# Kernel optimization log

Measured on AMD Instinct MI355X. Metric: run time of the kernel, lower is better.

The kernel has to match this reference:

```python
import jax, jax.numpy as jnp
import numpy as np

N = 20000; E = 320000; IN = 128; H = 6; C = 64; HC = H * C; NC = 16; NG = 64


def _gatv2(x, src, dst, wl, bl, wr, br, att, bias, heads, out_c, concat):
    # PyG GATv2Conv (eval mode, share_weights=False, negative_slope=0.2)
    n = x.shape[0]
    xl = (x @ wl + bl).reshape(n, heads, out_c)   # source-side transform
    xr = (x @ wr + br).reshape(n, heads, out_c)   # target-side transform
    # edge-wise attention logits: leaky_relu(x_l[j] + x_r[i]) . att
    e = jnp.einsum('ehc,hc->eh', jax.nn.leaky_relu(xl[src] + xr[dst], 0.2), att)
    # segment softmax over incoming edges of each target node
    emax = jax.ops.segment_max(e, dst, num_segments=n)
    a = jnp.exp(e - emax[dst])
    denom = jax.ops.segment_sum(a, dst, num_segments=n)
    alpha = a / (denom[dst] + 1e-16)
    out = jax.ops.segment_sum(xl[src] * alpha[:, :, None], dst, num_segments=n)
    out = out.reshape(n, heads * out_c) if concat else out.mean(axis=1)
    return out + bias


def setup_inputs() -> dict:
    key = jax.random.key(0)
    ks = jax.random.split(key, 32)
    s = 0.05
    inp = {}
    inp['x'] = jax.random.normal(ks[0], (N, IN), jnp.float32)
    inp['edge_index'] = jax.random.randint(ks[1], (2, E), 0, N, dtype=jnp.int32)
    inp['batch'] = jnp.sort(jax.random.randint(ks[2], (N,), 0, NG, dtype=jnp.int32))
    # input projection (input_dim != hidden_dim * n_heads)
    inp['inp_w'] = jax.random.normal(ks[3], (IN, HC), jnp.float32) * s
    inp['inp_b'] = jnp.zeros((HC,), jnp.float32)
    # layer 0: IN -> (H, C), concat
    inp['l0_wl'] = jax.random.normal(ks[4], (IN, HC), jnp.float32) * s
    inp['l0_bl'] = jnp.zeros((HC,), jnp.float32)
    inp['l0_wr'] = jax.random.normal(ks[5], (IN, HC), jnp.float32) * s
    inp['l0_br'] = jnp.zeros((HC,), jnp.float32)
    inp['l0_att'] = jax.random.normal(ks[6], (H, C), jnp.float32) * s
    inp['l0_bias'] = jnp.zeros((HC,), jnp.float32)
    # layer 1: HC -> (H, C), concat
    inp['l1_wl'] = jax.random.normal(ks[7], (HC, HC), jnp.float32) * s
    inp['l1_bl'] = jnp.zeros((HC,), jnp.float32)
    inp['l1_wr'] = jax.random.normal(ks[8], (HC, HC), jnp.float32) * s
    inp['l1_br'] = jnp.zeros((HC,), jnp.float32)
    inp['l1_att'] = jax.random.normal(ks[9], (H, C), jnp.float32) * s
    inp['l1_bias'] = jnp.zeros((HC,), jnp.float32)
    # layer 2: HC -> (1, C), no concat (mean over the single head)
    inp['l2_wl'] = jax.random.normal(ks[10], (HC, C), jnp.float32) * s
    inp['l2_bl'] = jnp.zeros((C,), jnp.float32)
    inp['l2_wr'] = jax.random.normal(ks[11], (HC, C), jnp.float32) * s
    inp['l2_br'] = jnp.zeros((C,), jnp.float32)
    inp['l2_att'] = jax.random.normal(ks[12], (1, C), jnp.float32) * s
    inp['l2_bias'] = jnp.zeros((C,), jnp.float32)
    # residual projection HC -> C at the last layer (bias-free Linear)
    inp['res_w'] = jax.random.normal(ks[13], (HC, C), jnp.float32) * s
    # dense head: Linear(C,C) + BatchNorm1d(eval) + ReLU + Linear(C,NC)
    inp['d1_w'] = jax.random.normal(ks[14], (C, C), jnp.float32) * s
    inp['d1_b'] = jnp.zeros((C,), jnp.float32)
    inp['bn_g'] = jnp.ones((C,), jnp.float32)
    inp['bn_b'] = jnp.zeros((C,), jnp.float32)
    inp['bn_m'] = jnp.zeros((C,), jnp.float32)
    inp['bn_v'] = jnp.ones((C,), jnp.float32)
    inp['d2_w'] = jax.random.normal(ks[15], (C, NC), jnp.float32) * s
    inp['d2_b'] = jnp.zeros((NC,), jnp.float32)
    return inp


def reference(x, edge_index, batch, inp_w, inp_b,
              l0_wl, l0_bl, l0_wr, l0_br, l0_att, l0_bias,
              l1_wl, l1_bl, l1_wr, l1_br, l1_att, l1_bias,
              l2_wl, l2_bl, l2_wr, l2_br, l2_att, l2_bias,
              res_w, d1_w, d1_b, bn_g, bn_b, bn_m, bn_v, d2_w, d2_b):
    n = x.shape[0]
    sl = jnp.arange(n, dtype=edge_index.dtype)           # self-loops (PyG default)
    src = jnp.concatenate([edge_index[0], sl])
    dst = jnp.concatenate([edge_index[1], sl])
    x_res = x @ inp_w + inp_b
    h = jax.nn.elu(_gatv2(x, src, dst, l0_wl, l0_bl, l0_wr, l0_br, l0_att, l0_bias, H, C, True)) + x_res
    x_res = h
    h = jax.nn.elu(_gatv2(h, src, dst, l1_wl, l1_bl, l1_wr, l1_br, l1_att, l1_bias, H, C, True)) + x_res
    x_res = h
    h = jax.nn.elu(_gatv2(h, src, dst, l2_wl, l2_bl, l2_wr, l2_br, l2_att, l2_bias, 1, C, False)) + x_res @ res_w
    pooled = jax.ops.segment_sum(h, batch, num_segments=NG)
    z = pooled @ d1_w + d1_b
    z = (z - bn_m) / jnp.sqrt(bn_v + 1e-5) * bn_g + bn_b  # BatchNorm1d eval
    z = jax.nn.relu(z) @ d2_w + d2_b
    return h, z
```

## Files before the change

### kernel.cpp

```cpp
#include <hip/hip_runtime.h>
#include <hip/hip_bf16.h>
#include <math.h>

#define NN 20000
#define EE 320000
#define IND 128
#define HH 6
#define CC 64
#define HCC 384
#define NCC 16
#define NGG 64

typedef __bf16 bf16x8 __attribute__((ext_vector_type(8)));
typedef float f32x4 __attribute__((ext_vector_type(4)));
typedef float f32x2 __attribute__((ext_vector_type(2)));
typedef unsigned short ushort_t;
typedef unsigned int uint_t;

#define LOG2E 1.44269504088896f

__device__ inline ushort_t f2bf(float f) {
    union { float f; uint_t u; } x; x.f = f;
    uint_t r = (x.u + 0x7FFF + ((x.u >> 16) & 1)) >> 16;
    return (ushort_t)r;
}
__device__ inline void bf8cvt2(uint4 v, f32x2* f) {
    union { uint_t u; float x; } a, b;
    a.u = v.x << 16; b.u = v.x & 0xFFFF0000u; f[0] = (f32x2){a.x, b.x};
    a.u = v.y << 16; b.u = v.y & 0xFFFF0000u; f[1] = (f32x2){a.x, b.x};
    a.u = v.z << 16; b.u = v.z & 0xFFFF0000u; f[2] = (f32x2){a.x, b.x};
    a.u = v.w << 16; b.u = v.w & 0xFFFF0000u; f[3] = (f32x2){a.x, b.x};
}

template <int CTRL>
__device__ inline float dppadd(float x) {
    int y = __builtin_amdgcn_mov_dpp(__builtin_bit_cast(int, x), CTRL, 0xF, 0xF, true);
    return x + __builtin_bit_cast(float, y);
}

__device__ inline void load_lds16(const ushort_t* g, ushort_t* l) {
    __builtin_amdgcn_global_load_lds(
        (const __attribute__((address_space(1))) void*)g,
        (__attribute__((address_space(3))) void*)l, 16, 0, 0);
}


__global__ void zero_init_kernel(int* counts, int* srcs_tail, int n) {
    int t = blockIdx.x * blockDim.x + threadIdx.x;
    if (t < n) counts[t] = 0;
    if (t < 8) srcs_tail[t] = 0;
}

__global__ void count_kernel(const int* __restrict__ ei, int* __restrict__ counts, int E) {
    int t = blockIdx.x * blockDim.x + threadIdx.x;
    if (t < E) atomicAdd(&counts[ei[E + t]], 1);
}

__global__ void scan_kernel(const int* __restrict__ counts, int* __restrict__ offsets,
                            int* __restrict__ cursor, int n) {
    __shared__ int part[1024];
    int t = threadIdx.x;
    int per = (n + 1023) / 1024;
    int base = t * per;
    int sum = 0;
    for (int j = 0; j < per; ++j) {
        int idx = base + j;
        if (idx < n) sum += counts[idx] + 1;
    }
    part[t] = sum;
    __syncthreads();
    for (int off = 1; off < 1024; off <<= 1) {
        int v = (t >= off) ? part[t - off] : 0;
        __syncthreads();
        part[t] += v;
        __syncthreads();
    }
    int run = (t == 0) ? 0 : part[t - 1];
    for (int j = 0; j < per; ++j) {
        int idx = base + j;
        if (idx < n) {
            int deg = counts[idx] + 1;
            offsets[idx] = run;
            cursor[idx] = run;
            run += deg;
        }
    }
    if (t == 1023) offsets[n] = part[1023];
}

__global__ void fill_kernel(const int* __restrict__ ei, int* __restrict__ cursor,
                            int* __restrict__ srcs, int E, int n) {
    int t = blockIdx.x * blockDim.x + threadIdx.x;
    if (t < E) {
        int s = ei[t];
        int d = ei[E + t];
        int slot = atomicAdd(&cursor[d], 1);
        srcs[slot] = s;
    } else if (t < E + n) {
        int i = t - E;
        int slot = atomicAdd(&cursor[i], 1);
        srcs[slot] = i;
    }
}

#define WBIG (1152 * IND)
#define WC1 (768 * HCC)
#define WC2 (192 * HCC)
#define XB_N (NN * IND)
#define PREP_TOTAL (WBIG + WC1 + WC2 + XB_N + 1152 + 768 + 192)

__global__ void prep_kernel(const float* __restrict__ x, const float* __restrict__ inp_w,
    const float* __restrict__ l0wl, const float* __restrict__ l0wr,
    const float* __restrict__ l1wl, const float* __restrict__ l1wr,
    const float* __restrict__ l2wl, const float* __restrict__ l2wr,
    const float* __restrict__ resw,
    const float* __restrict__ inp_b,
    const float* __restrict__ l0bl, const float* __restrict__ l0br,
    const float* __restrict__ l1bl, const float* __restrict__ l1br,
    const float* __restrict__ l2bl, const float* __restrict__ l2br,
    ushort_t* wBig, ushort_t* wC1, ushort_t* wC2, ushort_t* xb,
    float* bBig, float* bC1, float* bC2)
{
    int i = blockIdx.x * blockDim.x + threadIdx.x;
    if (i >= PREP_TOTAL) return;
    if (i < WBIG) {
        int col = i >> 7, k = i & 127;
        float v;
        if (col < 384)      v = inp_w[k * 384 + col];
        else if (col < 768) v = l0wl[k * 384 + (col - 384)];
        else                v = l0wr[k * 384 + (col - 768)];
        wBig[i] = f2bf(v); return;
    }
    i -= WBIG;
    if (i < WC1) {
        int col = i / 384, k = i - col * 384;
        float v = col < 384 ? l1wl[k * 384 + col] : l1wr[k * 384 + (col - 384)];
        wC1[i] = f2bf(v); return;
    }
    i -= WC1;
    if (i < WC2) {
        int col = i / 384, k = i - col * 384;
        float v;
        if (col < 64)       v = resw[k * 64 + col];
        else if (col < 128) v = l2wl[k * 64 + (col - 64)];
        else                v = l2wr[k * 64 + (col - 128)];
        wC2[i] = f2bf(v); return;
    }
    i -= WC2;
    if (i < XB_N) { xb[i] = f2bf(x[i]); return; }
    i -= XB_N;
    if (i < 1152) {
        float v;
        if (i < 384)      v = inp_b[i];
        else if (i < 768) v = l0bl[i - 384];
        else              v = l0br[i - 768];
        bBig[i] = v; return;
    }
    i -= 1152;
    if (i < 768) { bC1[i] = i < 384 ? l1bl[i] : l1br[i - 384]; return; }
    i -= 768;
    if (i < 192) {
        float v;
        if (i < 64)       v = 0.0f;
        else if (i < 128) v = l2bl[i - 64];
        else              v = l2br[i - 128];
        bC2[i] = v; return;
    }
}

__global__ __launch_bounds__(256) void gemm_mfma(
    const ushort_t* __restrict__ A, const ushort_t* __restrict__ BT,
    const float* __restrict__ bias,
    float* __restrict__ Cf, ushort_t* __restrict__ Cb1, int ld1,
    ushort_t* __restrict__ Cb2, int ld2, int split,
    int M, int N, int K)
{
    __shared__ ushort_t Bs[2][2][128 * 32];
    int t = threadIdx.x;
    int w = t >> 6, L = t & 63;
    int m0 = blockIdx.x * 128, n0 = blockIdx.y * 128;
    int q = L >> 4, r16 = L & 15;

    f32x4 acc[2][8];
#pragma unroll
    for (int a = 0; a < 2; ++a)
#pragma unroll
        for (int b = 0; b < 8; ++b) acc[a][b] = (f32x4){0.f, 0.f, 0.f, 0.f};

    int lr = L >> 2;
    int lc = ((L & 3) ^ ((lr >> 1) & 3)) * 8;
    int rB0 = min(n0 + w * 32 + lr, N - 1);
    int rB1 = min(n0 + w * 32 + 16 + lr, N - 1);
    const ushort_t* gB0 = BT + (size_t)rB0 * K + lc;
    const ushort_t* gB1 = BT + (size_t)rB1 * K + lc;
    int oB0 = (w * 32) * 32;
    int oB1 = (w * 32 + 16) * 32;

    int rA0 = min(m0 + w * 32 + r16, M - 1);
    int rA1 = min(m0 + w * 32 + 16 + r16, M - 1);
    const ushort_t* pA0 = A + (size_t)rA0 * K + q * 8;
    const ushort_t* pA1 = A + (size_t)rA1 * K + q * 8;

    int sw = (q ^ ((r16 >> 1) & 3)) * 8;

    load_lds16(gB0, &Bs[0][0][oB0]);
    load_lds16(gB1, &Bs[0][0][oB1]);
    load_lds16(gB0 + 32, &Bs[0][1][oB0]);
    load_lds16(gB1 + 32, &Bs[0][1][oB1]);
    gB0 += 64; gB1 += 64;
    bf16x8 a0 = *(const bf16x8*)pA0;
    bf16x8 a2 = *(const bf16x8*)(pA0 + 32);
    bf16x8 a1 = *(const bf16x8*)pA1;
    bf16x8 a3 = *(const bf16x8*)(pA1 + 32);
    pA0 += 64; pA1 += 64;

    int buf = 0;
    for (int k0 = 0; k0 < K; k0 += 64) {
        __syncthreads();
        bool more = (k0 + 64 < K);
        if (more) {
            int nb = buf ^ 1;
            load_lds16(gB0, &Bs[nb][0][oB0]);
            load_lds16(gB1, &Bs[nb][0][oB1]);
            load_lds16(gB0 + 32, &Bs[nb][1][oB0]);
            load_lds16(gB1 + 32, &Bs[nb][1][oB1]);
            gB0 += 64; gB1 += 64;
        }
        bf16x8 na0, na1, na2, na3;
        if (more) {
            na0 = *(const bf16x8*)pA0;
            na2 = *(const bf16x8*)(pA0 + 32);
            na1 = *(const bf16x8*)pA1;
            na3 = *(const bf16x8*)(pA1 + 32);
            pA0 += 64; pA1 += 64;
        }
#pragma unroll
        for (int ct = 0; ct < 8; ++ct) {
            bf16x8 blo = *(const bf16x8*)&Bs[buf][0][(ct * 16 + r16) * 32 + sw];
            bf16x8 bhi = *(const bf16x8*)&Bs[buf][1][(ct * 16 + r16) * 32 + sw];
            acc[0][ct] = __builtin_amdgcn_mfma_f32_16x16x32_bf16(blo, a0, acc[0][ct], 0, 0, 0);
            acc[1][ct] = __builtin_amdgcn_mfma_f32_16x16x32_bf16(blo, a1, acc[1][ct], 0, 0, 0);
            acc[0][ct] = __builtin_amdgcn_mfma_f32_16x16x32_bf16(bhi, a2, acc[0][ct], 0, 0, 0);
            acc[1][ct] = __builtin_amdgcn_mfma_f32_16x16x32_bf16(bhi, a3, acc[1][ct], 0, 0, 0);
        }
        if (more) { a0 = na0; a1 = na1; a2 = na2; a3 = na3; }
        buf ^= 1;
    }
#pragma unroll
    for (int rt = 0; rt < 2; ++rt) {
        int row = m0 + w * 32 + rt * 16 + r16;
        if (row >= M) continue;
#pragma unroll
        for (int ct = 0; ct < 8; ++ct) {
            int colb = n0 + ct * 16 + q * 4;
            if (colb >= N) continue;
            float4 bv = *(const float4*)(bias + colb);
            float v0 = acc[rt][ct][0] + bv.x;
            float v1 = acc[rt][ct][1] + bv.y;
            float v2 = acc[rt][ct][2] + bv.z;
            float v3 = acc[rt][ct][3] + bv.w;
            if (colb < split) {
                if (Cf) {
                    *(float4*)(Cf + (size_t)row * ld1 + colb) = make_float4(v0, v1, v2, v3);
                } else {
                    uint2 pk;
                    pk.x = (uint_t)f2bf(v0) | ((uint_t)f2bf(v1) << 16);
                    pk.y = (uint_t)f2bf(v2) | ((uint_t)f2bf(v3) << 16);
                    *(uint2*)(Cb1 + (size_t)row * ld1 + colb) = pk;
                }
            } else {
                uint2 pk;
                pk.x = (uint_t)f2bf(v0) | ((uint_t)f2bf(v1) << 16);
                pk.y = (uint_t)f2bf(v2) | ((uint_t)f2bf(v3) << 16);
                *(uint2*)(Cb2 + (size_t)row * ld2 + (colb - split)) = pk;
            }
        }
    }
}

__global__ __launch_bounds__(128) void gat6_kernel(
    const ushort_t* __restrict__ cat, const float* __restrict__ att,
    const float* __restrict__ bias, const ushort_t* __restrict__ resB,
    ushort_t* __restrict__ outB,
    const int* __restrict__ offsets, const int* __restrict__ srcs, int n)
{
    int wid = (blockIdx.x * blockDim.x + threadIdx.x) >> 6;
    if (wid >= n) return;
    int lane = threadIdx.x & 63;
    int h = lane >> 3, c8 = lane & 7;
    bool hv = h < HH;
    int off = h * 64 + c8 * 8;
    int offL = hv ? off : off - 384;
    int i = wid;
    int beg = offsets[i], end = offsets[i + 1];
    int deg = end - beg;
    int P = (deg + 1) >> 1;

    f32x2 xr2[4], att2[4];
    {
        uint4 v = *(const uint4*)(cat + (size_t)i * 768 + 384 + offL);
        bf8cvt2(v, xr2);
    }
#pragma unroll
    for (int j = 0; j < 4; ++j)
        att2[j] = (f32x2){att[offL + 2 * j] * LOG2E, att[offL + 2 * j + 1] * LOG2E};

    float s = 0.0f;
    f32x2 acc2[4];
#pragma unroll
    for (int j = 0; j < 4; ++j) acc2[j] = (f32x2){0.f, 0.f};

    int ia0 = srcs[beg], ib0 = srcs[beg + 1];
    uint4 cA = *(const uint4*)(cat + (size_t)ia0 * 768 + offL);
    uint4 cB = *(const uint4*)(cat + (size_t)ib0 * 768 + offL);
    int iA1 = srcs[beg + 2], iB1 = srcs[beg + 3];

    for (int p = 0; p < P; ++p) {
        uint4 nA = cA, nB = cB;
        bool pre = (p + 1 < P);
        if (pre) {
            nA = *(const uint4*)(cat + (size_t)iA1 * 768 + offL);
            nB = *(const uint4*)(cat + (size_t)iB1 * 768 + offL);
            iA1 = srcs[beg + 2 * p + 4];
            iB1 = srcs[beg + 2 * p + 5];
        }
        f32x2 xlA[4], xlB[4];
        bf8cvt2(cA, xlA);
        bf8cvt2(cB, xlB);
        f32x2 pA2 = (f32x2){0.f, 0.f}, pB2 = (f32x2){0.f, 0.f};
#pragma unroll
        for (int j = 0; j < 4; ++j) {
            f32x2 ta = xlA[j] + xr2[j];
            ta = __builtin_elementwise_max(ta, ta * 0.2f);
            pA2 += ta * att2[j];
            f32x2 tb = xlB[j] + xr2[j];
            tb = __builtin_elementwise_max(tb, tb * 0.2f);
            pB2 += tb * att2[j];
        }
        float pA = pA2.x + pA2.y, pB = pB2.x + pB2.y;
        pA = dppadd<0xB1>(pA);
        pB = dppadd<0xB1>(pB);
        pA = dppadd<0x4E>(pA);
        pB = dppadd<0x4E>(pB);
        pA = dppadd<0x141>(pA);
        pB = dppadd<0x141>(pB);
        float wA = __builtin_amdgcn_exp2f(pA);
        float wB = (2 * p + 1 < deg) ? __builtin_amdgcn_exp2f(pB) : 0.0f;
        s += wA + wB;
        f32x2 wA2 = (f32x2){wA, wA}, wB2 = (f32x2){wB, wB};
#pragma unroll
        for (int j = 0; j < 4; ++j) {
            acc2[j] += wA2 * xlA[j];
            acc2[j] += wB2 * xlB[j];
        }
        cA = nA; cB = nB;
    }

    if (hv) {
        float inv = 1.0f / (s + 1e-16f);
        size_t ob = (size_t)i * HCC + off;
        uint4 rv = *(const uint4*)(resB + ob);
        f32x2 rr[4];
        bf8cvt2(rv, rr);
        ushort_t u[8];
#pragma unroll
        for (int j = 0; j < 4; ++j) {
            float v0 = acc2[j].x * inv + bias[off + 2 * j];
            float v1 = acc2[j].y * inv + bias[off + 2 * j + 1];
            v0 = v0 > 0.0f ? v0 : expm1f(v0);
            v1 = v1 > 0.0f ? v1 : expm1f(v1);
            u[2 * j]     = f2bf(v0 + rr[j].x);
            u[2 * j + 1] = f2bf(v1 + rr[j].y);
        }
        *(uint4*)(outB + ob) = *(uint4*)u;
    }
}

__global__ __launch_bounds__(128) void gat1_kernel(
    const ushort_t* __restrict__ cat, const float* __restrict__ att,
    const float* __restrict__ bias, const float* __restrict__ res,
    float* __restrict__ out,
    const int* __restrict__ offsets, const int* __restrict__ srcs, int n)
{
    int wid = (blockIdx.x * blockDim.x + threadIdx.x) >> 6;
    if (wid >= n) return;
    int lane = threadIdx.x & 63;
    int e8 = lane >> 3, c8 = lane & 7;
    int i = wid;
    int beg = offsets[i], end = offsets[i + 1];

    f32x2 xr2[4], att2[4];
    {
        uint4 v = *(const uint4*)(cat + (size_t)i * 128 + 64 + c8 * 8);
        bf8cvt2(v, xr2);
    }
#pragma unroll
    for (int j = 0; j < 4; ++j)
        att2[j] = (f32x2){att[c8 * 8 + 2 * j] * LOG2E, att[c8 * 8 + 2 * j + 1] * LOG2E};

    float s = 0.0f;
    f32x2 acc2[4];
#pragma unroll
    for (int j = 0; j < 4; ++j) acc2[j] = (f32x2){0.f, 0.f};

    const uint4 z = make_uint4(0u, 0u, 0u, 0u);
    int p = beg + e8;
    bool val = p < end;
    int sj = val ? srcs[p] : i;
    uint4 v = *(const uint4*)(cat + (size_t)sj * 128 + c8 * 8);

    for (int p0 = beg; p0 < end; p0 += 8) {
        uint4 nv = z;
        bool nval = false;
        if (p0 + 8 < end) {
            int np = p0 + 8 + e8;
            nval = np < end;
            int nsj = nval ? srcs[np] : i;
            nv = *(const uint4*)(cat + (size_t)nsj * 128 + c8 * 8);
        }
        f32x2 xl[4];
        bf8cvt2(v, xl);
        f32x2 pp2 = (f32x2){0.f, 0.f};
#pragma unroll
        for (int j = 0; j < 4; ++j) {
            f32x2 tv = xl[j] + xr2[j];
            tv = __builtin_elementwise_max(tv, tv * 0.2f);
            pp2 += tv * att2[j];
        }
        float partial = pp2.x + pp2.y;
        partial = dppadd<0xB1>(partial);
        partial = dppadd<0x4E>(partial);
        partial = dppadd<0x141>(partial);
        float wE = val ? __builtin_amdgcn_exp2f(partial) : 0.0f;
        s += wE;
        f32x2 w2 = (f32x2){wE, wE};
#pragma unroll
        for (int j = 0; j < 4; ++j) acc2[j] += w2 * xl[j];
        v = nv;
        val = nval;
    }

    s = dppadd<0x140>(s);
    s += __shfl_xor(s, 16, 64);
    s += __shfl_xor(s, 32, 64);
#pragma unroll
    for (int j = 0; j < 4; ++j) {
        acc2[j].x += __shfl_xor(acc2[j].x, 8, 64);
        acc2[j].y += __shfl_xor(acc2[j].y, 8, 64);
        acc2[j].x += __shfl_xor(acc2[j].x, 16, 64);
        acc2[j].y += __shfl_xor(acc2[j].y, 16, 64);
        acc2[j].x += __shfl_xor(acc2[j].x, 32, 64);
        acc2[j].y += __shfl_xor(acc2[j].y, 32, 64);
    }
    if (e8 == 0) {
        float inv = 1.0f / (s + 1e-16f);
        size_t ob = (size_t)i * CC + c8 * 8;
        float4 r0 = *(const float4*)(res + ob);
        float4 r1 = *(const float4*)(res + ob + 4);
        float rr[8] = {r0.x, r0.y, r0.z, r0.w, r1.x, r1.y, r1.z, r1.w};
        float av[8] = {acc2[0].x, acc2[0].y, acc2[1].x, acc2[1].y,
                       acc2[2].x, acc2[2].y, acc2[3].x, acc2[3].y};
#pragma unroll
        for (int j = 0; j < 8; ++j) {
            float v2 = av[j] * inv + bias[c8 * 8 + j];
            v2 = v2 > 0.0f ? v2 : expm1f(v2);
            av[j] = v2 + rr[j];
        }
        *(float4*)(out + ob) = make_float4(av[0], av[1], av[2], av[3]);
        *(float4*)(out + ob + 4) = make_float4(av[4], av[5], av[6], av[7]);
    }
}

__global__ __launch_bounds__(256) void pool_kernel(const float* __restrict__ h,
                                                   const int* __restrict__ batch,
                                                   float* __restrict__ pooled, int n) {
    int g = blockIdx.x;
    int t = threadIdx.x;
    int w = t >> 6, lane = t & 63;
    int lo = 0, hi = n;
    while (lo < hi) { int mid = (lo + hi) >> 1; if (batch[mid] < g) lo = mid + 1; else hi = mid; }
    int start = lo;
    int hi2 = n;
    while (lo < hi2) { int mid = (lo + hi2) >> 1; if (batch[mid] < g + 1) lo = mid + 1; else hi2 = mid; }
    int endd = lo;
    float acc = 0.0f;
    for (int r = start + w; r < endd; r += 4)
        acc += h[(size_t)r * 64 + lane];
    __shared__ float red[4][64];
    red[w][lane] = acc;
    __syncthreads();
    if (w == 0)
        pooled[g * 64 + lane] = red[0][lane] + red[1][lane] + red[2][lane] + red[3][lane];
}

__global__ void head_kernel(const float* __restrict__ pooled,
                            const float* __restrict__ d1w, const float* __restrict__ d1b,
                            const float* __restrict__ bng, const float* __restrict__ bnb,
                            const float* __restrict__ bnm, const float* __restrict__ bnv,
                            const float* __restrict__ d2w, const float* __restrict__ d2b,
                            float* __restrict__ zout) {
    __shared__ float z1[64 * 64];
    int t = threadIdx.x;
    for (int idx = t; idx < 64 * 64; idx += 256) {
        int r = idx >> 6, c = idx & 63;
        float acc = d1b[c];
        for (int k = 0; k < 64; ++k) acc += pooled[r * 64 + k] * d1w[k * 64 + c];
        acc = (acc - bnm[c]) / sqrtf(bnv[c] + 1e-5f) * bng[c] + bnb[c];
        z1[idx] = acc > 0.0f ? acc : 0.0f;
    }
    __syncthreads();
    for (int idx = t; idx < 64 * NCC; idx += 256) {
        int r = idx >> 4, c = idx & 15;
        float acc = d2b[c];
        for (int k = 0; k < 64; ++k) acc += z1[r * 64 + k] * d2w[k * NCC + c];
        zout[idx] = acc;
    }
}


extern "C" void kernel_launch(void* const* d_in, const int* in_sizes, int n_in,
                              void* d_out, int out_size, void* d_ws, size_t ws_size,
                              hipStream_t stream) {
    const int N = NN, E = EE, C = CC, HC = HCC, NG = NGG;
    const int EN = E + N;

    const float* x     = (const float*)d_in[0];
    const int*   ei    = (const int*)d_in[1];
    const int*   batch = (const int*)d_in[2];
    const float* inp_w = (const float*)d_in[3];
    const float* inp_b = (const float*)d_in[4];
    const float* l0_wl = (const float*)d_in[5];
    const float* l0_bl = (const float*)d_in[6];
    const float* l0_wr = (const float*)d_in[7];
    const float* l0_br = (const float*)d_in[8];
    const float* l0_att = (const float*)d_in[9];
    const float* l0_bias = (const float*)d_in[10];
    const float* l1_wl = (const float*)d_in[11];
    const float* l1_bl = (const float*)d_in[12];
    const float* l1_wr = (const float*)d_in[13];
    const float* l1_br = (const float*)d_in[14];
    const float* l1_att = (const float*)d_in[15];
    const float* l1_bias = (const float*)d_in[16];
    const float* l2_wl = (const float*)d_in[17];
    const float* l2_bl = (const float*)d_in[18];
    const float* l2_wr = (const float*)d_in[19];
    const float* l2_br = (const float*)d_in[20];
    const float* l2_att = (const float*)d_in[21];
    const float* l2_bias = (const float*)d_in[22];
    const float* res_w = (const float*)d_in[23];
    const float* d1_w = (const float*)d_in[24];
    const float* d1_b = (const float*)d_in[25];
    const float* bn_g = (const float*)d_in[26];
    const float* bn_b = (const float*)d_in[27];
    const float* bn_m = (const float*)d_in[28];
    const float* bn_v = (const float*)d_in[29];
    const float* d2_w = (const float*)d_in[30];
    const float* d2_b = (const float*)d_in[31];

    float* out = (float*)d_out;

    char* ws = (char*)d_ws;
    size_t off = 0;
    auto alloc = [&](size_t bytes) -> void* {
        void* p = ws + off;
        off += (bytes + 255) & ~(size_t)255;
        return p;
    };
    ushort_t* bufH_b  = (ushort_t*)alloc((size_t)N * HC * 2);
    ushort_t* cat01_b = (ushort_t*)alloc((size_t)N * 768 * 2 + 2048);
    ushort_t* xres_b  = (ushort_t*)alloc((size_t)N * HC * 2);
    ushort_t* cat2_b  = (ushort_t*)alloc((size_t)N * 128 * 2);
    float*    bufRes  = (float*)alloc((size_t)N * C * 4);
    ushort_t* xb      = (ushort_t*)alloc((size_t)N * IND * 2);
    ushort_t* wBig    = (ushort_t*)alloc((size_t)WBIG * 2);
    ushort_t* wC1     = (ushort_t*)alloc((size_t)WC1 * 2);
    ushort_t* wC2     = (ushort_t*)alloc((size_t)WC2 * 2);
    float*    bBig    = (float*)alloc((size_t)1152 * 4);
    float*    bC1     = (float*)alloc((size_t)768 * 4);
    float*    bC2     = (float*)alloc((size_t)192 * 4);
    int*      counts  = (int*)alloc((size_t)N * 4);
    int*      cursor  = (int*)alloc((size_t)N * 4);
    int*      offsets = (int*)alloc((size_t)(N + 1) * 4);
    int*      srcs    = (int*)alloc((size_t)(EN + 8) * 4);
    float*    pooled  = (float*)alloc((size_t)NG * C * 4);

    zero_init_kernel<<<(N + 255) / 256, 256, 0, stream>>>(counts, srcs + EN, N);
    count_kernel<<<(E + 255) / 256, 256, 0, stream>>>(ei, counts, E);
    scan_kernel<<<1, 1024, 0, stream>>>(counts, offsets, cursor, N);
    fill_kernel<<<(EN + 255) / 256, 256, 0, stream>>>(ei, cursor, srcs, E, N);
    prep_kernel<<<(PREP_TOTAL + 255) / 256, 256, 0, stream>>>(
        x, inp_w, l0_wl, l0_wr, l1_wl, l1_wr, l2_wl, l2_wr, res_w,
        inp_b, l0_bl, l0_br, l1_bl, l1_br, l2_bl, l2_br,
        wBig, wC1, wC2, xb, bBig, bC1, bC2);

    dim3 blk(256);
    int mtiles = (N + 127) / 128;
    dim3 gblk(128);
    int gatBlocks = (N * 64 + 127) / 128;

    gemm_mfma<<<dim3(mtiles, 9), blk, 0, stream>>>(xb, wBig, bBig,
        nullptr, xres_b, HC, cat01_b, 768, 384, N, 1152, IND);
    gat6_kernel<<<gatBlocks, gblk, 0, stream>>>(cat01_b, l0_att, l0_bias,
                                                xres_b, bufH_b, offsets, srcs, N);
    gemm_mfma<<<dim3(mtiles, 6), blk, 0, stream>>>(bufH_b, wC1, bC1,
        nullptr, nullptr, 0, cat01_b, 768, 0, N, 768, HC);
    gat6_kernel<<<gatBlocks, gblk, 0, stream>>>(cat01_b, l1_att, l1_bias,
                                                bufH_b, bufH_b, offsets, srcs, N);
    gemm_mfma<<<dim3(mtiles, 2), blk, 0, stream>>>(bufH_b, wC2, bC2,
        bufRes, nullptr, C, cat2_b, 128, 64, N, 192, HC);
    gat1_kernel<<<gatBlocks, gblk, 0, stream>>>(cat2_b, l2_att, l2_bias,
                                                bufRes, out, offsets, srcs, N);
    pool_kernel<<<NG, 256, 0, stream>>>(out, batch, pooled, N);
    head_kernel<<<1, 256, 0, stream>>>(pooled, d1_w, d1_b, bn_g, bn_b, bn_m, bn_v,
                                       d2_w, d2_b, out + (size_t)N * C);
}
```

Baseline: 429.9 us.

## Add 256-row multi-N-tile GEMM, precompute byte offsets, LDS-buffered scan

Adds a new 512-thread GEMM kernel that covers 256 rows per block and loops over several 128-column tiles, so each block reuses its A rows across column tiles and fewer blocks are launched for the first two projections. The fill kernel now stores source indices pre-scaled to byte offsets in two separate arrays, one per gather row stride, which removes the multiply in the gather loops. Edge offsets are loaded through readfirstlane so they live in scalar registers. The scan kernel stages the counts in LDS and writes offsets with coalesced accesses. In exchange it writes a second index array, uses a large LDS buffer in the scan, and runs fewer, heavier GEMM blocks that could lower occupancy.

```diff
diff --git a/kernel.cpp b/kernel.cpp
--- a/kernel.cpp
+++ b/kernel.cpp
@@ -45,10 +45,10 @@
 }
 
 
-__global__ void zero_init_kernel(int* counts, int* srcs_tail, int n) {
+__global__ void zero_init_kernel(int* counts, int* s6_tail, int* s1_tail, int n) {
     int t = blockIdx.x * blockDim.x + threadIdx.x;
     if (t < n) counts[t] = 0;
-    if (t < 8) srcs_tail[t] = 0;
+    if (t < 8) { s6_tail[t] = 0; s1_tail[t] = 0; }
 }
 
 __global__ void count_kernel(const int* __restrict__ ei, int* __restrict__ counts, int E) {
@@ -56,16 +56,20 @@
     if (t < E) atomicAdd(&counts[ei[E + t]], 1);
 }
 
-__global__ void scan_kernel(const int* __restrict__ counts, int* __restrict__ offsets,
-                            int* __restrict__ cursor, int n) {
+__global__ __launch_bounds__(1024) void scan_kernel(
+    const int* __restrict__ counts, int* __restrict__ offsets,
+    int* __restrict__ cursor, int n) {
+    __shared__ int buf[NN];
     __shared__ int part[1024];
     int t = threadIdx.x;
+    for (int idx = t; idx < n; idx += 1024) buf[idx] = counts[idx] + 1;
+    __syncthreads();
     int per = (n + 1023) / 1024;
     int base = t * per;
     int sum = 0;
     for (int j = 0; j < per; ++j) {
         int idx = base + j;
-        if (idx < n) sum += counts[idx] + 1;
+        if (idx < n) sum += buf[idx];
     }
     part[t] = sum;
     __syncthreads();
@@ -79,27 +83,35 @@
     for (int j = 0; j < per; ++j) {
         int idx = base + j;
         if (idx < n) {
-            int deg = counts[idx] + 1;
-            offsets[idx] = run;
-            cursor[idx] = run;
+            int deg = buf[idx];
+            buf[idx] = run;
             run += deg;
         }
     }
-    if (t == 1023) offsets[n] = part[1023];
+    __syncthreads();
+    for (int idx = t; idx < n; idx += 1024) {
+        int v = buf[idx];
+        offsets[idx] = v;
+        cursor[idx] = v;
+    }
+    if (t == 1023) offsets[n] = run;
 }
 
 __global__ void fill_kernel(const int* __restrict__ ei, int* __restrict__ cursor,
-                            int* __restrict__ srcs, int E, int n) {
+                            int* __restrict__ srcs6, int* __restrict__ srcs1,
+                            int E, int n) {
     int t = blockIdx.x * blockDim.x + threadIdx.x;
     if (t < E) {
         int s = ei[t];
         int d = ei[E + t];
         int slot = atomicAdd(&cursor[d], 1);
-        srcs[slot] = s;
+        srcs6[slot] = s * 1536;
+        srcs1[slot] = s << 8;
     } else if (t < E + n) {
         int i = t - E;
         int slot = atomicAdd(&cursor[i], 1);
-        srcs[slot] = i;
+        srcs6[slot] = i * 1536;
+        srcs1[slot] = i << 8;
     }
 }
 
@@ -165,6 +177,101 @@
         else if (i < 128) v = l2bl[i - 64];
         else              v = l2br[i - 128];
         bC2[i] = v; return;
+    }
+}
+
+__global__ __launch_bounds__(512) void gemm_mfma2(
+    const ushort_t* __restrict__ A, const ushort_t* __restrict__ BT,
+    const float* __restrict__ bias,
+    ushort_t* __restrict__ Cb1, int ld1,
+    ushort_t* __restrict__ Cb2, int ld2, int split,
+    int M, int N, int K, int NT)
+{
+    __shared__ ushort_t Bs[2][2][128 * 32];
+    int t = threadIdx.x;
+    int w = t >> 6, L = t & 63;
+    int m0 = blockIdx.x * 256;
+    int q = L >> 4, r16 = L & 15;
+    int lr = L >> 2;
+    int lc = ((L & 3) ^ ((lr >> 1) & 3)) * 8;
+    int sw = (q ^ ((r16 >> 1) & 3)) * 8;
+    int oB = (w * 16) * 32;
+
+    int rA0 = min(m0 + w * 32 + r16, M - 1);
+    int rA1 = min(m0 + w * 32 + 16 + r16, M - 1);
+    const ushort_t* pA0base = A + (size_t)rA0 * K + q * 8;
+    const ushort_t* pA1base = A + (size_t)rA1 * K + q * 8;
+
+    for (int nt = 0; nt < NT; ++nt) {
+        int n0 = (blockIdx.y * NT + nt) * 128;
+        int rB = min(n0 + w * 16 + lr, N - 1);
+        const ushort_t* gB = BT + (size_t)rB * K + lc;
+        const ushort_t* pA0 = pA0base;
+        const ushort_t* pA1 = pA1base;
+
+        f32x4 acc[2][8];
+#pragma unroll
+        for (int a = 0; a < 2; ++a)
+#pragma unroll
+            for (int b = 0; b < 8; ++b) acc[a][b] = (f32x4){0.f, 0.f, 0.f, 0.f};
+
+        load_lds16(gB, &Bs[0][0][oB]);
+        load_lds16(gB + 32, &Bs[0][1][oB]);
+        gB += 64;
+        bf16x8 a0 = *(const bf16x8*)pA0;
+        bf16x8 a2 = *(const bf16x8*)(pA0 + 32);
+        bf16x8 a1 = *(const bf16x8*)pA1;
+        bf16x8 a3 = *(const bf16x8*)(pA1 + 32);
+        pA0 += 64; pA1 += 64;
+
+        int buf = 0;
+        for (int k0 = 0; k0 < K; k0 += 64) {
+            __syncthreads();
+            bool more = (k0 + 64 < K);
+            if (more) {
+                int nb = buf ^ 1;
+                load_lds16(gB, &Bs[nb][0][oB]);
+                load_lds16(gB + 32, &Bs[nb][1][oB]);
+                gB += 64;
+            }
+            bf16x8 na0, na1, na2, na3;
+            if (more) {
+                na0 = *(const bf16x8*)pA0;
+                na2 = *(const bf16x8*)(pA0 + 32);
+                na1 = *(const bf16x8*)pA1;
+                na3 = *(const bf16x8*)(pA1 + 32);
+                pA0 += 64; pA1 += 64;
+            }
+#pragma unroll
+            for (int ct = 0; ct < 8; ++ct) {
+                bf16x8 blo = *(const bf16x8*)&Bs[buf][0][(ct * 16 + r16) * 32 + sw];
+                bf16x8 bhi = *(const bf16x8*)&Bs[buf][1][(ct * 16 + r16) * 32 + sw];
+                acc[0][ct] = __builtin_amdgcn_mfma_f32_16x16x32_bf16(blo, a0, acc[0][ct], 0, 0, 0);
+                acc[1][ct] = __builtin_amdgcn_mfma_f32_16x16x32_bf16(blo, a1, acc[1][ct], 0, 0, 0);
+                acc[0][ct] = __builtin_amdgcn_mfma_f32_16x16x32_bf16(bhi, a2, acc[0][ct], 0, 0, 0);
+                acc[1][ct] = __builtin_amdgcn_mfma_f32_16x16x32_bf16(bhi, a3, acc[1][ct], 0, 0, 0);
+            }
+            if (more) { a0 = na0; a1 = na1; a2 = na2; a3 = na3; }
+            buf ^= 1;
+        }
+#pragma unroll
+        for (int rt = 0; rt < 2; ++rt) {
+            int row = m0 + w * 32 + rt * 16 + r16;
+            if (row >= M) continue;
+#pragma unroll
+            for (int ct = 0; ct < 8; ++ct) {
+                int colb = n0 + ct * 16 + q * 4;
+                if (colb >= N) continue;
+                float4 bv = *(const float4*)(bias + colb);
+                uint2 pk;
+                pk.x = (uint_t)f2bf(acc[rt][ct][0] + bv.x) | ((uint_t)f2bf(acc[rt][ct][1] + bv.y) << 16);
+                pk.y = (uint_t)f2bf(acc[rt][ct][2] + bv.z) | ((uint_t)f2bf(acc[rt][ct][3] + bv.w) << 16);
+                if (colb < split)
+                    *(uint2*)(Cb1 + (size_t)row * ld1 + colb) = pk;
+                else
+                    *(uint2*)(Cb2 + (size_t)row * ld2 + (colb - split)) = pk;
+            }
+        }
     }
 }
 
@@ -282,7 +389,7 @@
     const ushort_t* __restrict__ cat, const float* __restrict__ att,
     const float* __restrict__ bias, const ushort_t* __restrict__ resB,
     ushort_t* __restrict__ outB,
-    const int* __restrict__ offsets, const int* __restrict__ srcs, int n)
+    const int* __restrict__ offsets, const int* __restrict__ srcs6, int n)
 {
     int wid = (blockIdx.x * blockDim.x + threadIdx.x) >> 6;
     if (wid >= n) return;
@@ -290,39 +397,43 @@
     int h = lane >> 3, c8 = lane & 7;
     bool hv = h < HH;
     int off = h * 64 + c8 * 8;
-    int offL = hv ? off : off - 384;
+    int offL2 = (hv ? off : off - 384) * 2;
     int i = wid;
-    int beg = offsets[i], end = offsets[i + 1];
+    int beg = __builtin_amdgcn_readfirstlane(offsets[i]);
+    int end = __builtin_amdgcn_readfirstlane(offsets[i + 1]);
     int deg = end - beg;
     int P = (deg + 1) >> 1;
+    const char* catc = (const char*)cat;
 
     f32x2 xr2[4], att2[4];
     {
-        uint4 v = *(const uint4*)(cat + (size_t)i * 768 + 384 + offL);
+        uint4 v = *(const uint4*)(catc + (size_t)i * 1536 + 768 + offL2);
         bf8cvt2(v, xr2);
     }
 #pragma unroll
-    for (int j = 0; j < 4; ++j)
-        att2[j] = (f32x2){att[offL + 2 * j] * LOG2E, att[offL + 2 * j + 1] * LOG2E};
+    for (int j = 0; j < 4; ++j) {
+        int o = (offL2 >> 1) + 2 * j;
+        att2[j] = (f32x2){att[o] * LOG2E, att[o + 1] * LOG2E};
+    }
 
     float s = 0.0f;
     f32x2 acc2[4];
 #pragma unroll
     for (int j = 0; j < 4; ++j) acc2[j] = (f32x2){0.f, 0.f};
 
-    int ia0 = srcs[beg], ib0 = srcs[beg + 1];
-    uint4 cA = *(const uint4*)(cat + (size_t)ia0 * 768 + offL);
-    uint4 cB = *(const uint4*)(cat + (size_t)ib0 * 768 + offL);
-    int iA1 = srcs[beg + 2], iB1 = srcs[beg + 3];
+    int bA0 = srcs6[beg], bB0 = srcs6[beg + 1];
+    uint4 cA = *(const uint4*)(catc + (size_t)(uint_t)bA0 + offL2);
+    uint4 cB = *(const uint4*)(catc + (size_t)(uint_t)bB0 + offL2);
+    int iA1 = srcs6[beg + 2], iB1 = srcs6[beg + 3];
 
     for (int p = 0; p < P; ++p) {
         uint4 nA = cA, nB = cB;
         bool pre = (p + 1 < P);
         if (pre) {
-            nA = *(const uint4*)(cat + (size_t)iA1 * 768 + offL);
-            nB = *(const uint4*)(cat + (size_t)iB1 * 768 + offL);
-            iA1 = srcs[beg + 2 * p + 4];
-            iB1 = srcs[beg + 2 * p + 5];
+            nA = *(const uint4*)(catc + (size_t)(uint_t)iA1 + offL2);
+            nB = *(const uint4*)(catc + (size_t)(uint_t)iB1 + offL2);
+            iA1 = srcs6[beg + 2 * p + 4];
+            iB1 = srcs6[beg + 2 * p + 5];
         }
         f32x2 xlA[4], xlB[4];
         bf8cvt2(cA, xlA);
@@ -380,14 +491,16 @@
     const ushort_t* __restrict__ cat, const float* __restrict__ att,
     const float* __restrict__ bias, const float* __restrict__ res,
     float* __restrict__ out,
-    const int* __restrict__ offsets, const int* __restrict__ srcs, int n)
+    const int* __restrict__ offsets, const int* __restrict__ srcs1, int n)
 {
     int wid = (blockIdx.x * blockDim.x + threadIdx.x) >> 6;
     if (wid >= n) return;
     int lane = threadIdx.x & 63;
     int e8 = lane >> 3, c8 = lane & 7;
     int i = wid;
-    int beg = offsets[i], end = offsets[i + 1];
+    int beg = __builtin_amdgcn_readfirstlane(offsets[i]);
+    int end = __builtin_amdgcn_readfirstlane(offsets[i + 1]);
+    const char* catc = (const char*)cat;
 
     f32x2 xr2[4], att2[4];
     {
@@ -406,8 +519,8 @@
     const uint4 z = make_uint4(0u, 0u, 0u, 0u);
     int p = beg + e8;
     bool val = p < end;
-    int sj = val ? srcs[p] : i;
-    uint4 v = *(const uint4*)(cat + (size_t)sj * 128 + c8 * 8);
+    int b = val ? srcs1[p] : (i << 8);
+    uint4 v = *(const uint4*)(catc + (size_t)(uint_t)b + c8 * 16);
 
     for (int p0 = beg; p0 < end; p0 += 8) {
         uint4 nv = z;
@@ -415,8 +528,8 @@
         if (p0 + 8 < end) {
             int np = p0 + 8 + e8;
             nval = np < end;
-            int nsj = nval ? srcs[np] : i;
-            nv = *(const uint4*)(cat + (size_t)nsj * 128 + c8 * 8);
+            int nb = nval ? srcs1[np] : (i << 8);
+            nv = *(const uint4*)(catc + (size_t)(uint_t)nb + c8 * 16);
         }
         f32x2 xl[4];
         bf8cvt2(v, xl);
@@ -581,35 +694,36 @@
     int*      counts  = (int*)alloc((size_t)N * 4);
     int*      cursor  = (int*)alloc((size_t)N * 4);
     int*      offsets = (int*)alloc((size_t)(N + 1) * 4);
-    int*      srcs    = (int*)alloc((size_t)(EN + 8) * 4);
+    int*      srcs6   = (int*)alloc((size_t)(EN + 8) * 4);
+    int*      srcs1   = (int*)alloc((size_t)(EN + 8) * 4);
     float*    pooled  = (float*)alloc((size_t)NG * C * 4);
 
-    zero_init_kernel<<<(N + 255) / 256, 256, 0, stream>>>(counts, srcs + EN, N);
+    zero_init_kernel<<<(N + 255) / 256, 256, 0, stream>>>(counts, srcs6 + EN, srcs1 + EN, N);
     count_kernel<<<(E + 255) / 256, 256, 0, stream>>>(ei, counts, E);
     scan_kernel<<<1, 1024, 0, stream>>>(counts, offsets, cursor, N);
-    fill_kernel<<<(EN + 255) / 256, 256, 0, stream>>>(ei, cursor, srcs, E, N);
+    fill_kernel<<<(EN + 255) / 256, 256, 0, stream>>>(ei, cursor, srcs6, srcs1, E, N);
     prep_kernel<<<(PREP_TOTAL + 255) / 256, 256, 0, stream>>>(
         x, inp_w, l0_wl, l0_wr, l1_wl, l1_wr, l2_wl, l2_wr, res_w,
         inp_b, l0_bl, l0_br, l1_bl, l1_br, l2_bl, l2_br,
         wBig, wC1, wC2, xb, bBig, bC1, bC2);
 
-    dim3 blk(256);
+    int mtiles256 = (N + 255) / 256;
     int mtiles = (N + 127) / 128;
     dim3 gblk(128);
     int gatBlocks = (N * 64 + 127) / 128;
 
-    gemm_mfma<<<dim3(mtiles, 9), blk, 0, stream>>>(xb, wBig, bBig,
-        nullptr, xres_b, HC, cat01_b, 768, 384, N, 1152, IND);
+    gemm_mfma2<<<dim3(mtiles256, 3), dim3(512), 0, stream>>>(xb, wBig, bBig,
+        xres_b, HC, cat01_b, 768, 384, N, 1152, IND, 3);
     gat6_kernel<<<gatBlocks, gblk, 0, stream>>>(cat01_b, l0_att, l0_bias,
-                                                xres_b, bufH_b, offsets, srcs, N);
-    gemm_mfma<<<dim3(mtiles, 6), blk, 0, stream>>>(bufH_b, wC1, bC1,
-        nullptr, nullptr, 0, cat01_b, 768, 0, N, 768, HC);
+                                                xres_b, bufH_b, offsets, srcs6, N);
+    gemm_mfma2<<<dim3(mtiles256, 3), dim3(512), 0, stream>>>(bufH_b, wC1, bC1,
+        nullptr, 0, cat01_b, 768, 0, N, 768, HC, 2);
     gat6_kernel<<<gatBlocks, gblk, 0, stream>>>(cat01_b, l1_att, l1_bias,
-                                                bufH_b, bufH_b, offsets, srcs, N);
-    gemm_mfma<<<dim3(mtiles, 2), blk, 0, stream>>>(bufH_b, wC2, bC2,
+                                                bufH_b, bufH_b, offsets, srcs6, N);
+    gemm_mfma<<<dim3(mtiles, 2), dim3(256), 0, stream>>>(bufH_b, wC2, bC2,
         bufRes, nullptr, C, cat2_b, 128, 64, N, 192, HC);
     gat1_kernel<<<gatBlocks, gblk, 0, stream>>>(cat2_b, l2_att, l2_bias,
-                                                bufRes, out, offsets, srcs, N);
+                                                bufRes, out, offsets, srcs1, N);
     pool_kernel<<<NG, 256, 0, stream>>>(out, batch, pooled, N);
     head_kernel<<<1, 256, 0, stream>>>(pooled, d1_w, d1_b, bn_g, bn_b, bn_m, bn_v,
                                        d2_w, d2_b, out + (size_t)N * C);
```

New measurement: 428.6 us. No clear change (-0.3%).
